# Optimization experiments

Measured on AMD Instinct MI355X. Metric: run time of the kernel, lower is better.

The kernel has to match this reference:

```python
import jax, jax.numpy as jnp
import numpy as np

RES = 128          # image / k-space resolution
DECIMATION = 4     # acceleration factor
P = RES * RES // DECIMATION  # 4096 trajectory points
B = 8              # batch


def setup_inputs() -> dict:
    key = jax.random.key(0)
    k1, k2 = jax.random.split(key)
    k_space_input = jax.random.normal(k1, (B, 1, RES, RES, 2), dtype=jnp.float32)
    # learnable k-space trajectory in pixel units, range [-RES/2, RES/2]
    trajectory = (jax.random.uniform(k2, (P, 2), dtype=jnp.float32) - 0.5) * RES
    return {"k_space_input": k_space_input, "trajectory": trajectory}


def _grid_sample_points(img, pts_norm):
    """torch.nn.functional.grid_sample (bilinear, zero padding, align_corners=False)
    evaluated at a list of points.
    img: (B, C, H, W); pts_norm: (P, 2) in [-1, 1], [:, 0] -> x (W axis), [:, 1] -> y (H axis).
    Returns (B, C, P)."""
    H, W = img.shape[-2], img.shape[-1]
    x = (pts_norm[:, 0] + 1.0) * (W * 0.5) - 0.5
    y = (pts_norm[:, 1] + 1.0) * (H * 0.5) - 0.5
    x0f = jnp.floor(x)
    y0f = jnp.floor(y)
    wx = x - x0f  # differentiable interpolation weights
    wy = y - y0f
    x0 = x0f.astype(jnp.int32)
    y0 = y0f.astype(jnp.int32)

    def tap(ix, iy, w):
        valid = ((ix >= 0) & (ix < W) & (iy >= 0) & (iy < H)).astype(img.dtype)
        ixc = jnp.clip(ix, 0, W - 1)
        iyc = jnp.clip(iy, 0, H - 1)
        return img[:, :, iyc, ixc] * (w * valid)  # (B, C, P)

    return (tap(x0, y0, (1 - wx) * (1 - wy))
            + tap(x0 + 1, y0, wx * (1 - wy))
            + tap(x0, y0 + 1, (1 - wx) * wy)
            + tap(x0 + 1, y0 + 1, wx * wy))


def _forward(k_space_input, trajectory):
    # (B,1,H,W,2) -> (B,2,H,W): channels = (real, imag)
    ksp = jnp.transpose(k_space_input, (0, 1, 4, 2, 3))[:, 0]
    # bilinear resampling of cartesian k-space at the trajectory points
    pts = trajectory / (RES * 0.5)  # normalize to [-1, 1] as in the torch helper
    sub = _grid_sample_points(ksp, pts)            # (B, 2, P)
    c = sub[:, 0] + 1j * sub[:, 1]                 # complex measurements (B, P)
    # adjoint (type-1) NUFFT back to a centered RES x RES image grid:
    # img[y, x] = (1/RES) * sum_p c[p] * exp(+2*pi*i*(ky_p*y + kx_p*x)/RES)
    xs = jnp.arange(RES, dtype=jnp.float32) - RES * 0.5  # centered grid coords
    phase = (2.0 * jnp.pi / RES)
    Ax = jnp.exp(1j * phase * trajectory[:, 0][:, None] * xs[None, :])  # (P, W)
    Ay = jnp.exp(1j * phase * trajectory[:, 1][:, None] * xs[None, :])  # (P, H)
    tmp = c[:, :, None] * Ay[None, :, :]           # (B, P, H)
    img = jnp.einsum('bph,pw->bhw', tmp, Ax) / RES  # (B, H, W), 1/sqrt(H*W) scale
    out = jnp.stack([img.real, img.imag], axis=-1)[:, None]  # (B, 1, H, W, 2)
    return out


def reference(k_space_input, trajectory):
    return _forward(k_space_input, trajectory)
```

## Files before the change

kernel.cpp:

```cpp
#include <hip/hip_runtime.h>

#define RES    128
#define P_PTS  4096
#define BATCH  8
#define CHUNKS 16

#define BT_OFF   0u
#define AT_OFF   (2u * 1024u * 1024u)
#define PART_OFF (18u * 1024u * 1024u)

typedef _Float16 half8  __attribute__((ext_vector_type(8)));
typedef _Float16 half2v __attribute__((ext_vector_type(2)));
typedef float    f32x4  __attribute__((ext_vector_type(4)));

__device__ __forceinline__ float2 phasor(float rev) {
    const float f = rev - floorf(rev);
    return make_float2(__builtin_amdgcn_cosf(f), __builtin_amdgcn_sinf(f));
}

__device__ __forceinline__ void gload16(const void* g, void* lbase) {
    __builtin_amdgcn_global_load_lds(
        (const __attribute__((address_space(1))) void*)g,
        (__attribute__((address_space(3))) void*)lbase, 16, 0, 0);
}

__global__ __launch_bounds__(128) void prep_kernel(const float* __restrict__ ksp,
                                                   const float* __restrict__ traj,
                                                   _Float16* __restrict__ Bt,
                                                   _Float16* __restrict__ At) {
    const int k8 = blockIdx.x;
    const int t  = threadIdx.x;

    __shared__ float2 sc[4][8];

    if (t < 32) {
        const int j = t >> 3, b = t & 7;
        const int p = k8 * 4 + j;
        const float tx = traj[2 * p], ty = traj[2 * p + 1];
        const float x = tx + 63.5f, y = ty + 63.5f;
        const float x0f = floorf(x), y0f = floorf(y);
        const float wx = x - x0f, wy = y - y0f;
        const int ix0 = (int)x0f, iy0 = (int)y0f;
        float re = 0.0f, im = 0.0f;
#pragma unroll
        for (int dy = 0; dy < 2; ++dy) {
#pragma unroll
            for (int dx = 0; dx < 2; ++dx) {
                const int ix = ix0 + dx, iy = iy0 + dy;
                const float w = (dx ? wx : 1.0f - wx) * (dy ? wy : 1.0f - wy);
                if (ix >= 0 && ix < RES && iy >= 0 && iy < RES) {
                    const int base = ((b * RES + iy) * RES + ix) * 2;
                    re = fmaf(ksp[base],     w, re);
                    im = fmaf(ksp[base + 1], w, im);
                }
            }
        }
        sc[j][b] = make_float2(re * (1.0f / 128.0f), im * (1.0f / 128.0f));
    }
    __syncthreads();

    const float xs = ((float)t - 64.0f) * (1.0f / 128.0f);
    float2 ay[4];
    half8 bv;
#pragma unroll
    for (int j = 0; j < 4; ++j) {
        const int p = k8 * 4 + j;
        const float2 ax = phasor(traj[2 * p] * xs);
        ay[j] = phasor(traj[2 * p + 1] * xs);
        bv[2 * j]     = (_Float16)ax.x;
        bv[2 * j + 1] = (_Float16)ax.y;
    }
    *(half8*)(Bt + ((size_t)k8 * 128 + t) * 8) = bv;

#pragma unroll
    for (int b = 0; b < 8; ++b) {
        half8 v;
#pragma unroll
        for (int j = 0; j < 4; ++j) {
            const float cr = sc[j][b].x, ci = sc[j][b].y;
            v[2 * j]     = (_Float16)(cr * ay[j].x - ci * ay[j].y);
            v[2 * j + 1] = (_Float16)(cr * ay[j].y + ci * ay[j].x);
        }
        *(half8*)(At + (((size_t)b * 1024 + k8) * 128 + t) * 8) = v;
    }
}

__global__ __launch_bounds__(256) void gemm_kernel(const _Float16* __restrict__ At,
                                                   const _Float16* __restrict__ Bt,
                                                   half2v* __restrict__ part) {
    __shared__ __align__(16) _Float16 sA[2][4096];
    __shared__ __align__(16) _Float16 sB[2][8192];

    const int chunk = blockIdx.x;
    const int mt_   = blockIdx.y;
    const int b  = mt_ >> 1;
    const int mh = mt_ & 1;
    const int tid  = threadIdx.x;
    const int wave = tid >> 6;
    const int lane = tid & 63;
    const int l15  = lane & 15;
    const int q    = lane >> 4;

    const _Float16* aCh = At + ((size_t)b * 1024 + chunk * 64) * 1024 + mh * 512;
    const _Float16* bCh = Bt + (size_t)chunk * 64 * 1024;

    const half8 SGN = {(_Float16)1.f, (_Float16)-1.f, (_Float16)1.f, (_Float16)-1.f,
                       (_Float16)1.f, (_Float16)-1.f, (_Float16)1.f, (_Float16)-1.f};

    f32x4 accR[4][2], accI[4][2];
#pragma unroll
    for (int i = 0; i < 4; ++i)
#pragma unroll
        for (int j = 0; j < 2; ++j) {
            accR[i][j] = (f32x4){0.f, 0.f, 0.f, 0.f};
            accI[i][j] = (f32x4){0.f, 0.f, 0.f, 0.f};
        }

    auto stage = [&](int r, int buf) {
#pragma unroll
        for (int i = 0; i < 2; ++i) {
            const int k8l = wave * 2 + i;
            const size_t k8o = (size_t)(r * 8 + k8l) * 1024;
            gload16(aCh + k8o + lane * 8, &sA[buf][k8l * 512]);
            gload16(bCh + k8o + lane * 8, &sB[buf][k8l * 1024]);
            gload16(bCh + k8o + 512 + lane * 8, &sB[buf][k8l * 1024 + 512]);
        }
    };

    auto compute = [&](int buf) {
#pragma unroll
        for (int s = 0; s < 2; ++s) {
            const _Float16* pa = &sA[buf][(s * 4 + q) * 512];
            const _Float16* pb = &sB[buf][(s * 4 + q) * 1024];
            half8 an[4], bv[2], a1[4], a2[4];
#pragma unroll
            for (int mt = 0; mt < 4; ++mt)
                an[mt] = *(const half8*)(pa + (mt * 16 + l15) * 8);
#pragma unroll
            for (int nt = 0; nt < 2; ++nt)
                bv[nt] = *(const half8*)(pb + (wave * 32 + nt * 16 + l15) * 8);
#pragma unroll
            for (int mt = 0; mt < 4; ++mt) {
                a1[mt] = an[mt] * SGN;
                a2[mt] = __builtin_shufflevector(an[mt], an[mt],
                                                 1, 0, 3, 2, 5, 4, 7, 6);
            }
#pragma unroll
            for (int mt = 0; mt < 4; ++mt)
#pragma unroll
                for (int nt = 0; nt < 2; ++nt) {
                    accR[mt][nt] = __builtin_amdgcn_mfma_f32_16x16x32_f16(
                        a1[mt], bv[nt], accR[mt][nt], 0, 0, 0);
                    accI[mt][nt] = __builtin_amdgcn_mfma_f32_16x16x32_f16(
                        a2[mt], bv[nt], accI[mt][nt], 0, 0, 0);
                }
        }
    };

    stage(0, 0);
#pragma unroll
    for (int r = 0; r < 8; ++r) {
        if (r < 7) {
            stage(r + 1, (r + 1) & 1);
            asm volatile("s_waitcnt vmcnt(6)\n\ts_barrier" ::: "memory");
        } else {
            asm volatile("s_waitcnt vmcnt(0)\n\ts_barrier" ::: "memory");
        }
        compute(r & 1);
        asm volatile("s_waitcnt lgkmcnt(0)\n\ts_barrier" ::: "memory");
    }

#pragma unroll
    for (int mt = 0; mt < 4; ++mt) {
#pragma unroll
        for (int nt = 0; nt < 2; ++nt) {
            const int n = wave * 32 + nt * 16 + l15;
#pragma unroll
            for (int rg = 0; rg < 4; ++rg) {
                const int m = b * 128 + mh * 64 + mt * 16 + q * 4 + rg;
                half2v pv;
                pv[0] = (_Float16)accR[mt][nt][rg];
                pv[1] = (_Float16)accI[mt][nt][rg];
                part[(size_t)chunk * 131072 + m * 128 + n] = pv;
            }
        }
    }
}

__global__ __launch_bounds__(256) void reduce_kernel(const half2v* __restrict__ part,
                                                     float2* __restrict__ out) {
    const int i = blockIdx.x * 256 + threadIdx.x;
    float sr = 0.f, si = 0.f;
#pragma unroll
    for (int c = 0; c < CHUNKS; ++c) {
        half2v v = part[(size_t)c * 131072 + i];
        sr += (float)v[0];
        si += (float)v[1];
    }
    out[i] = make_float2(sr, si);
}

extern "C" void kernel_launch(void* const* d_in, const int* in_sizes, int n_in,
                              void* d_out, int out_size, void* d_ws, size_t ws_size,
                              hipStream_t stream) {
    const float* ksp  = (const float*)d_in[0];
    const float* traj = (const float*)d_in[1];

    _Float16* Bt   = (_Float16*)((char*)d_ws + BT_OFF);
    _Float16* At   = (_Float16*)((char*)d_ws + AT_OFF);
    half2v*   part = (half2v*)((char*)d_ws + PART_OFF);

    hipLaunchKernelGGL(prep_kernel,   dim3(1024),        dim3(128), 0, stream,
                       ksp, traj, Bt, At);
    hipLaunchKernelGGL(gemm_kernel,   dim3(CHUNKS, 16),  dim3(256), 0, stream,
                       At, Bt, part);
    hipLaunchKernelGGL(reduce_kernel, dim3(512),         dim3(256), 0, stream,
                       part, (float2*)d_out);
}
```

Measured before the change: 79.64 us.

## Fuse prep into GEMM by generating phasor tiles on the fly in LDS

Removes the separate prep kernel and its ~18MB of global fp16 A/B intermediates. Each GEMM block now samples k-space for its 256 points and computes the cos/sin phasor tiles directly into shared memory before each MFMA step. This trades global memory traffic and a launch for redundant transcendental work, since every block recomputes B tiles and the interpolation. It also drops the double-buffered async global-to-LDS pipeline in favour of synchronous compute, then barrier, then MFMA.

```diff
diff --git a/kernel.cpp b/kernel.cpp
--- a/kernel.cpp
+++ b/kernel.cpp
@@ -2,41 +2,34 @@
 
 #define RES    128
 #define P_PTS  4096
-#define BATCH  8
 #define CHUNKS 16
-
-#define BT_OFF   0u
-#define AT_OFF   (2u * 1024u * 1024u)
-#define PART_OFF (18u * 1024u * 1024u)
+#define PP     256
 
 typedef _Float16 half8  __attribute__((ext_vector_type(8)));
 typedef _Float16 half2v __attribute__((ext_vector_type(2)));
 typedef float    f32x4  __attribute__((ext_vector_type(4)));
 
-__device__ __forceinline__ float2 phasor(float rev) {
-    const float f = rev - floorf(rev);
-    return make_float2(__builtin_amdgcn_cosf(f), __builtin_amdgcn_sinf(f));
-}
+__global__ __launch_bounds__(256) void gemm_kernel(const float* __restrict__ ksp,
+                                                   const float* __restrict__ traj,
+                                                   half2v* __restrict__ part) {
+    __shared__ float2 st[PP];
+    __shared__ float2 sc[PP];
+    __shared__ __align__(16) _Float16 sA[4096];
+    __shared__ __align__(16) _Float16 sB[8192];
 
-__device__ __forceinline__ void gload16(const void* g, void* lbase) {
-    __builtin_amdgcn_global_load_lds(
-        (const __attribute__((address_space(1))) void*)g,
-        (__attribute__((address_space(3))) void*)lbase, 16, 0, 0);
-}
+    const int chunk = blockIdx.x;
+    const int b     = blockIdx.y >> 1;
+    const int mh    = blockIdx.y & 1;
+    const int tid   = threadIdx.x;
+    const int wave  = tid >> 6;
+    const int lane  = tid & 63;
+    const int l15   = lane & 15;
+    const int q     = lane >> 4;
 
-__global__ __launch_bounds__(128) void prep_kernel(const float* __restrict__ ksp,
-                                                   const float* __restrict__ traj,
-                                                   _Float16* __restrict__ Bt,
-                                                   _Float16* __restrict__ At) {
-    const int k8 = blockIdx.x;
-    const int t  = threadIdx.x;
-
-    __shared__ float2 sc[4][8];
-
-    if (t < 32) {
-        const int j = t >> 3, b = t & 7;
-        const int p = k8 * 4 + j;
+    {
+        const int p = chunk * PP + tid;
         const float tx = traj[2 * p], ty = traj[2 * p + 1];
+        st[tid] = make_float2(tx, ty);
         const float x = tx + 63.5f, y = ty + 63.5f;
         const float x0f = floorf(x), y0f = floorf(y);
         const float wx = x - x0f, wy = y - y0f;
@@ -49,63 +42,15 @@
                 const int ix = ix0 + dx, iy = iy0 + dy;
                 const float w = (dx ? wx : 1.0f - wx) * (dy ? wy : 1.0f - wy);
                 if (ix >= 0 && ix < RES && iy >= 0 && iy < RES) {
-                    const int base = ((b * RES + iy) * RES + ix) * 2;
-                    re = fmaf(ksp[base],     w, re);
-                    im = fmaf(ksp[base + 1], w, im);
+                    const float2 v = *(const float2*)(ksp + ((b * RES + iy) * RES + ix) * 2);
+                    re = fmaf(v.x, w, re);
+                    im = fmaf(v.y, w, im);
                 }
             }
         }
-        sc[j][b] = make_float2(re * (1.0f / 128.0f), im * (1.0f / 128.0f));
+        sc[tid] = make_float2(re * (1.0f / 128.0f), im * (1.0f / 128.0f));
     }
     __syncthreads();
-
-    const float xs = ((float)t - 64.0f) * (1.0f / 128.0f);
-    float2 ay[4];
-    half8 bv;
-#pragma unroll
-    for (int j = 0; j < 4; ++j) {
-        const int p = k8 * 4 + j;
-        const float2 ax = phasor(traj[2 * p] * xs);
-        ay[j] = phasor(traj[2 * p + 1] * xs);
-        bv[2 * j]     = (_Float16)ax.x;
-        bv[2 * j + 1] = (_Float16)ax.y;
-    }
-    *(half8*)(Bt + ((size_t)k8 * 128 + t) * 8) = bv;
-
-#pragma unroll
-    for (int b = 0; b < 8; ++b) {
-        half8 v;
-#pragma unroll
-        for (int j = 0; j < 4; ++j) {
-            const float cr = sc[j][b].x, ci = sc[j][b].y;
-            v[2 * j]     = (_Float16)(cr * ay[j].x - ci * ay[j].y);
-            v[2 * j + 1] = (_Float16)(cr * ay[j].y + ci * ay[j].x);
-        }
-        *(half8*)(At + (((size_t)b * 1024 + k8) * 128 + t) * 8) = v;
-    }
-}
-
-__global__ __launch_bounds__(256) void gemm_kernel(const _Float16* __restrict__ At,
-                                                   const _Float16* __restrict__ Bt,
-                                                   half2v* __restrict__ part) {
-    __shared__ __align__(16) _Float16 sA[2][4096];
-    __shared__ __align__(16) _Float16 sB[2][8192];
-
-    const int chunk = blockIdx.x;
-    const int mt_   = blockIdx.y;
-    const int b  = mt_ >> 1;
-    const int mh = mt_ & 1;
-    const int tid  = threadIdx.x;
-    const int wave = tid >> 6;
-    const int lane = tid & 63;
-    const int l15  = lane & 15;
-    const int q    = lane >> 4;
-
-    const _Float16* aCh = At + ((size_t)b * 1024 + chunk * 64) * 1024 + mh * 512;
-    const _Float16* bCh = Bt + (size_t)chunk * 64 * 1024;
-
-    const half8 SGN = {(_Float16)1.f, (_Float16)-1.f, (_Float16)1.f, (_Float16)-1.f,
-                       (_Float16)1.f, (_Float16)-1.f, (_Float16)1.f, (_Float16)-1.f};
 
     f32x4 accR[4][2], accI[4][2];
 #pragma unroll
@@ -116,22 +61,51 @@
             accI[i][j] = (f32x4){0.f, 0.f, 0.f, 0.f};
         }
 
-    auto stage = [&](int r, int buf) {
+    const float inv = 1.0f / 128.0f;
+    const int nB = tid & 127, kB = tid >> 7;
+    const int mA = tid & 63,  kA = tid >> 6;
+    const float xn = ((float)nB - 64.0f) * inv;
+    const float xm = ((float)(mh * 64 + mA) - 64.0f) * inv;
+
+    for (int r = 0; r < 8; ++r) {
+        const int p0 = r * 32;
+#pragma unroll
+        for (int i = 0; i < 4; ++i) {
+            const int k8l = kB + 2 * i;
+            half8 v;
+#pragma unroll
+            for (int j = 0; j < 4; ++j) {
+                const int pl = p0 + k8l * 4 + j;
+                const float rev = st[pl].x * xn;
+                const float f = rev - floorf(rev);
+                v[2 * j]     = (_Float16)__builtin_amdgcn_cosf(f);
+                v[2 * j + 1] = (_Float16)__builtin_amdgcn_sinf(f);
+            }
+            *(half8*)(sB + ((size_t)(k8l * 128 + nB)) * 8) = v;
+        }
 #pragma unroll
         for (int i = 0; i < 2; ++i) {
-            const int k8l = wave * 2 + i;
-            const size_t k8o = (size_t)(r * 8 + k8l) * 1024;
-            gload16(aCh + k8o + lane * 8, &sA[buf][k8l * 512]);
-            gload16(bCh + k8o + lane * 8, &sB[buf][k8l * 1024]);
-            gload16(bCh + k8o + 512 + lane * 8, &sB[buf][k8l * 1024 + 512]);
+            const int k8l = kA + 4 * i;
+            half8 v;
+#pragma unroll
+            for (int j = 0; j < 4; ++j) {
+                const int pl = p0 + k8l * 4 + j;
+                const float rev = st[pl].y * xm;
+                const float f = rev - floorf(rev);
+                const float cs = __builtin_amdgcn_cosf(f);
+                const float sn = __builtin_amdgcn_sinf(f);
+                const float cr = sc[pl].x, ci = sc[pl].y;
+                v[2 * j]     = (_Float16)(cr * cs - ci * sn);
+                v[2 * j + 1] = (_Float16)(cr * sn + ci * cs);
+            }
+            *(half8*)(sA + ((size_t)(k8l * 64 + mA)) * 8) = v;
         }
-    };
+        __syncthreads();
 
-    auto compute = [&](int buf) {
 #pragma unroll
         for (int s = 0; s < 2; ++s) {
-            const _Float16* pa = &sA[buf][(s * 4 + q) * 512];
-            const _Float16* pb = &sB[buf][(s * 4 + q) * 1024];
+            const _Float16* pa = sA + (s * 4 + q) * 512;
+            const _Float16* pb = sB + (s * 4 + q) * 1024;
             half8 an[4], bv[2], a1[4], a2[4];
 #pragma unroll
             for (int mt = 0; mt < 4; ++mt)
@@ -139,6 +113,8 @@
 #pragma unroll
             for (int nt = 0; nt < 2; ++nt)
                 bv[nt] = *(const half8*)(pb + (wave * 32 + nt * 16 + l15) * 8);
+            const half8 SGN = {(_Float16)1.f, (_Float16)-1.f, (_Float16)1.f, (_Float16)-1.f,
+                               (_Float16)1.f, (_Float16)-1.f, (_Float16)1.f, (_Float16)-1.f};
 #pragma unroll
             for (int mt = 0; mt < 4; ++mt) {
                 a1[mt] = an[mt] * SGN;
@@ -155,19 +131,7 @@
                         a2[mt], bv[nt], accI[mt][nt], 0, 0, 0);
                 }
         }
-    };
-
-    stage(0, 0);
-#pragma unroll
-    for (int r = 0; r < 8; ++r) {
-        if (r < 7) {
-            stage(r + 1, (r + 1) & 1);
-            asm volatile("s_waitcnt vmcnt(6)\n\ts_barrier" ::: "memory");
-        } else {
-            asm volatile("s_waitcnt vmcnt(0)\n\ts_barrier" ::: "memory");
-        }
-        compute(r & 1);
-        asm volatile("s_waitcnt lgkmcnt(0)\n\ts_barrier" ::: "memory");
+        __syncthreads();
     }
 
 #pragma unroll
@@ -205,15 +169,10 @@
                               hipStream_t stream) {
     const float* ksp  = (const float*)d_in[0];
     const float* traj = (const float*)d_in[1];
+    half2v* part = (half2v*)d_ws;
 
-    _Float16* Bt   = (_Float16*)((char*)d_ws + BT_OFF);
-    _Float16* At   = (_Float16*)((char*)d_ws + AT_OFF);
-    half2v*   part = (half2v*)((char*)d_ws + PART_OFF);
-
-    hipLaunchKernelGGL(prep_kernel,   dim3(1024),        dim3(128), 0, stream,
-                       ksp, traj, Bt, At);
-    hipLaunchKernelGGL(gemm_kernel,   dim3(CHUNKS, 16),  dim3(256), 0, stream,
-                       At, Bt, part);
-    hipLaunchKernelGGL(reduce_kernel, dim3(512),         dim3(256), 0, stream,
+    hipLaunchKernelGGL(gemm_kernel,   dim3(CHUNKS, 16), dim3(256), 0, stream,
+                       ksp, traj, part);
+    hipLaunchKernelGGL(reduce_kernel, dim3(512),        dim3(256), 0, stream,
                        part, (float2*)d_out);
 }
```

Result: faster. 74.37 us (-6.6%).
